# Kernel optimization log

Hardware: AMD Instinct MI355X
Metric: run time of the kernel (lower is better)

The kernel has to match this reference:

```python
import jax, jax.numpy as jnp
import numpy as np

N, E, D, H, HID = 50000, 400000, 64, 8, 1024
NEG_SLOPE = 0.2
BN_EPS = 1e-5


def setup_inputs() -> dict:
    key = jax.random.key(0)
    ks = jax.random.split(key, 10)
    s = 0.05
    return {
        "x": jax.random.normal(ks[0], (N, D), jnp.float32),
        "src": jax.random.randint(ks[1], (E,), 0, N, jnp.int32),
        "dst": jax.random.randint(ks[2], (E,), 0, N, jnp.int32),
        "fc_w": jax.random.normal(ks[3], (H * D, D), jnp.float32) * s,
        "attn_l": jax.random.normal(ks[4], (H, D), jnp.float32) * s,
        "attn_r": jax.random.normal(ks[5], (H, D), jnp.float32) * s,
        "gat_bias": jnp.zeros((H * D,), jnp.float32),
        "bn1_gamma": jnp.ones((H * D,), jnp.float32),
        "bn1_beta": jnp.zeros((H * D,), jnp.float32),
        "w1": jax.random.normal(ks[6], (HID, H * D), jnp.float32) * s,
        "b1": jnp.zeros((HID,), jnp.float32),
        "w2": jax.random.normal(ks[7], (D, HID), jnp.float32) * s,
        "b2": jnp.zeros((D,), jnp.float32),
        "bn2_gamma": jnp.ones((D,), jnp.float32),
        "bn2_beta": jnp.zeros((D,), jnp.float32),
    }


def _batchnorm(h, gamma, beta):
    # training-mode BatchNorm1d: batch statistics over node axis
    mu = h.mean(axis=0)
    var = h.var(axis=0)
    return gamma * (h - mu) * jax.lax.rsqrt(var + BN_EPS) + beta


def reference(x, src, dst, fc_w, attn_l, attn_r, gat_bias,
              bn1_gamma, bn1_beta, w1, b1, w2, b2, bn2_gamma, bn2_beta):
    n = x.shape[0]
    nh, dh = attn_l.shape
    # --- GATConv ---
    feat = (x @ fc_w.T).reshape(n, nh, dh)                 # [N,H,Dh]
    el = jnp.einsum("nhd,hd->nh", feat, attn_l)            # [N,H]
    er = jnp.einsum("nhd,hd->nh", feat, attn_r)            # [N,H]
    e = jax.nn.leaky_relu(el[src] + er[dst], NEG_SLOPE)    # [E,H]
    # edge softmax grouped by destination node (numerically stable)
    emax = jax.ops.segment_max(e, dst, num_segments=n)
    emax = jnp.where(jnp.isfinite(emax), emax, 0.0)        # nodes w/ no in-edges
    ez = jnp.exp(e - emax[dst])
    denom = jax.ops.segment_sum(ez, dst, num_segments=n)
    alpha = ez / denom[dst]                                # [E,H]
    msg = alpha[:, :, None] * feat[src]                    # [E,H,Dh]
    rst = jax.ops.segment_sum(msg, dst, num_segments=n)    # [N,H,Dh]
    rst = rst + gat_bias.reshape(nh, dh)
    h = rst.reshape(n, nh * dh)                            # flatten(1)
    # --- feed forward: BN -> Linear -> ReLU -> Linear -> BN ---
    h = _batchnorm(h, bn1_gamma, bn1_beta)
    h = jax.nn.relu(h @ w1.T + b1)
    h = h @ w2.T + b2
    h = _batchnorm(h, bn2_gamma, bn2_beta)
    return h
```

## Files before the change

kernel.cpp:

```cpp
#include <hip/hip_runtime.h>

#define NEG_SLOPE 0.2f
#define BN_EPS 1e-5f

typedef __bf16 bf16x8 __attribute__((ext_vector_type(8)));
typedef float  f32x4  __attribute__((ext_vector_type(4)));
typedef unsigned short ushort8_t __attribute__((ext_vector_type(8)));

__device__ __forceinline__ unsigned short f2bf(float f) {
    unsigned int u = __float_as_uint(f);
    unsigned int r = u + 0x7FFFu + ((u >> 16) & 1u);
    return (unsigned short)(r >> 16);
}
__device__ __forceinline__ float bf2f(unsigned short u) {
    return __uint_as_float(((unsigned int)u) << 16);
}
__device__ __forceinline__ void gload16(const void* g, void* l) {
    __builtin_amdgcn_global_load_lds(
        (const __attribute__((address_space(1))) unsigned int*)g,
        (__attribute__((address_space(3))) unsigned int*)l, 16, 0, 0);
}

__global__ __launch_bounds__(256)
void prep(const float* __restrict__ x, const int* __restrict__ dst,
          const float* __restrict__ fc_w, const float* __restrict__ w2,
          const float* __restrict__ attn_l, const float* __restrict__ attn_r,
          unsigned short* __restrict__ xbf, unsigned short* __restrict__ fcwbf,
          unsigned short* __restrict__ w2bf, float* __restrict__ proj,
          int* __restrict__ counts, int totX4, int E,
          int bCvtx, int bHist, int bFcw, int bW2)
{
    const int bid = blockIdx.x, tid = threadIdx.x;
    if (bid < bCvtx) {
        int i4 = bid * 256 + tid;
        if (i4 < totX4) {
            float4 v = *(const float4*)(x + (size_t)i4 * 4);
            ushort4 o = {f2bf(v.x), f2bf(v.y), f2bf(v.z), f2bf(v.w)};
            *(ushort4*)(xbf + (size_t)i4 * 4) = o;
        }
    } else if (bid < bHist) {
        int base = (bid - bCvtx) * 1024 + tid;
        #pragma unroll
        for (int k = 0; k < 4; ++k) {
            int e = base + k * 256;
            if (e < E) atomicAdd(&counts[dst[e]], 1);
        }
    } else if (bid < bFcw) {
        int i4 = (bid - bHist) * 256 + tid;
        if (i4 < 8192) {
            float4 v = *(const float4*)(fc_w + (size_t)i4 * 4);
            ushort4 o = {f2bf(v.x), f2bf(v.y), f2bf(v.z), f2bf(v.w)};
            *(ushort4*)(fcwbf + (size_t)i4 * 4) = o;
        }
    } else if (bid < bW2) {
        int i4 = (bid - bFcw) * 256 + tid;
        if (i4 < 16384) {
            float4 v = *(const float4*)(w2 + (size_t)i4 * 4);
            ushort4 o = {f2bf(v.x), f2bf(v.y), f2bf(v.z), f2bf(v.w)};
            *(ushort4*)(w2bf + (size_t)i4 * 4) = o;
        }
    } else {
        for (int t2 = tid; t2 < 512; t2 += 256) {
            int h = t2 >> 6, k = t2 & 63;
            float al = 0.f, ar = 0.f;
            for (int d = 0; d < 64; ++d) {
                float w = fc_w[(size_t)(h * 64 + d) * 64 + k];
                al = fmaf(attn_l[h * 64 + d], w, al);
                ar = fmaf(attn_r[h * 64 + d], w, ar);
            }
            proj[t2] = al;
            proj[512 + t2] = ar;
        }
    }
}

__global__ __launch_bounds__(256)
void scan1_elr(const int* __restrict__ counts, int* __restrict__ incl,
               int* __restrict__ bsum, int N, int NB,
               const float* __restrict__ x, const float* __restrict__ proj,
               float* __restrict__ el, float* __restrict__ er, int NH)
{
    __shared__ int sm[256];
    if ((int)blockIdx.x < NB) {
        int i = blockIdx.x * 256 + threadIdx.x;
        int v = (i < N) ? counts[i] : 0;
        sm[threadIdx.x] = v;
        __syncthreads();
        #pragma unroll
        for (int d = 1; d < 256; d <<= 1) {
            int t = (threadIdx.x >= d) ? sm[threadIdx.x - d] : 0;
            __syncthreads();
            sm[threadIdx.x] += t;
            __syncthreads();
        }
        if (i < N) incl[i] = sm[threadIdx.x];
        if (threadIdx.x == 255) bsum[blockIdx.x] = sm[255];
    } else {
        int idx = (blockIdx.x - NB) * 256 + threadIdx.x;
        if (idx >= NH) return;
        int h = idx & 7, n = idx >> 3;
        const float4* f  = (const float4*)(x + (size_t)n * 64);
        const float4* pl = (const float4*)(proj + h * 64);
        const float4* pr = (const float4*)(proj + 512 + h * 64);
        float sl = 0.f, sr = 0.f;
        #pragma unroll
        for (int i = 0; i < 16; ++i) {
            float4 fv = f[i], lv = pl[i], rv = pr[i];
            sl += fv.x * lv.x + fv.y * lv.y + fv.z * lv.z + fv.w * lv.w;
            sr += fv.x * rv.x + fv.y * rv.y + fv.z * rv.z + fv.w * rv.w;
        }
        el[idx] = sl;
        er[idx] = sr;
    }
}

__global__ void scan23(const int* __restrict__ incl, const int* __restrict__ bsum,
                       int* __restrict__ row_ptr, int* __restrict__ cursor, int N, int NB)
{
    __shared__ int sm[256];
    int t = threadIdx.x;
    sm[t] = (t < (int)blockIdx.x && t < NB) ? bsum[t] : 0;
    __syncthreads();
    #pragma unroll
    for (int d = 128; d > 0; d >>= 1) {
        if (t < d) sm[t] += sm[t + d];
        __syncthreads();
    }
    int pre = sm[0];
    int i = blockIdx.x * 256 + t;
    if (i < N) {
        int v = incl[i] + pre;
        row_ptr[i + 1] = v;
        cursor[i + 1] = v;
    }
    if (i == 0) { row_ptr[0] = 0; cursor[0] = 0; }
}

__global__ void scatter_edges(const int* __restrict__ src, const int* __restrict__ dst,
                              int* __restrict__ cursor, int* __restrict__ esrc, int E) {
    int e = blockIdx.x * 256 + threadIdx.x;
    if (e < E) {
        int p = atomicAdd(&cursor[dst[e]], 1);
        esrc[p] = src[e];
    }
}

__global__ __launch_bounds__(256)
void gat_aggregate(const int* __restrict__ row_ptr, const int* __restrict__ esrc,
                   const float* __restrict__ el, const float* __restrict__ er,
                   const unsigned short* __restrict__ xb, unsigned short* __restrict__ xagg,
                   int N)
{
    int node = blockIdx.x * 4 + (threadIdx.x >> 6);
    if (node >= N) return;
    const int lane = threadIdx.x & 63;
    const int h = lane >> 3, j = lane & 7;
    const int beg = row_ptr[node], end = row_ptr[node + 1];
    const float er_n = er[node * 8 + h];

    float denom = 0.f;
    float a[8] = {};
    int s_cur = (beg < end) ? esrc[beg] : 0;
    for (int k = beg; k < end; ++k) {
        int s_nxt = (k + 1 < end) ? esrc[k + 1] : 0;
        float elv = el[s_cur * 8 + h];
        ushort8_t fv = *(const ushort8_t*)(xb + (size_t)s_cur * 64 + j * 8);
        float v = elv + er_n;
        v = (v > 0.f) ? v : NEG_SLOPE * v;
        float z = __expf(v);
        denom += z;
        #pragma unroll
        for (int t = 0; t < 8; ++t) a[t] = fmaf(z, bf2f(fv[t]), a[t]);
        s_cur = s_nxt;
    }
    float inv = (end > beg) ? 1.f / denom : 0.f;
    ushort8_t o;
    #pragma unroll
    for (int t = 0; t < 8; ++t) o[t] = f2bf(a[t] * inv);
    *(ushort8_t*)(xagg + (size_t)node * 512 + lane * 8) = o;
}

__global__ __launch_bounds__(256)
void bn1_stats(const unsigned short* __restrict__ Xa,
               const unsigned short* __restrict__ Fw,
               const float* __restrict__ gat_bias,
               float* __restrict__ sums1, int M)
{
    __shared__ alignas(16) char Asm[128 * 64 * 2];
    __shared__ alignas(16) char Bsm[64 * 64 * 2];
    __shared__ float reds[4][64], redq[4][64];
    const int tid = threadIdx.x, lane = tid & 63, wave = tid >> 6;
    const int bm = blockIdx.x * 128;
    const int head = blockIdx.y;
    const int lr = lane >> 3, lk = ((lane & 7) ^ lr) * 8;

    #pragma unroll
    for (int it = 0; it < 4; ++it) {
        int seg = wave * 4 + it;
        gload16(Xa + (size_t)(bm + seg * 8 + lr) * 512 + head * 64 + lk, Asm + seg * 1024);
    }
    #pragma unroll
    for (int it = 0; it < 2; ++it) {
        int seg = wave * 2 + it;
        gload16(Fw + (size_t)(head * 64 + seg * 8 + lr) * 64 + lk, Bsm + seg * 1024);
    }
    __syncthreads();

    f32x4 acc[2][4] = {};
    #pragma unroll
    for (int kk = 0; kk < 2; ++kk) {
        int kg = kk * 4 + (lane >> 4);
        bf16x8 a[2], b[4];
        #pragma unroll
        for (int i = 0; i < 2; ++i) {
            int row = wave * 32 + i * 16 + (lane & 15);
            a[i] = *(const bf16x8*)(Asm + row * 128 + ((kg ^ (row & 7)) << 4));
        }
        #pragma unroll
        for (int j = 0; j < 4; ++j) {
            int row = j * 16 + (lane & 15);
            b[j] = *(const bf16x8*)(Bsm + row * 128 + ((kg ^ (row & 7)) << 4));
        }
        #pragma unroll
        for (int i = 0; i < 2; ++i)
            #pragma unroll
            for (int j = 0; j < 4; ++j)
                acc[i][j] = __builtin_amdgcn_mfma_f32_16x16x32_bf16(a[i], b[j], acc[i][j], 0, 0, 0);
    }

    float s4[4] = {}, q4[4] = {};
    #pragma unroll
    for (int j = 0; j < 4; ++j) {
        int col = j * 16 + (lane & 15);
        float bias = gat_bias[head * 64 + col];
        #pragma unroll
        for (int i = 0; i < 2; ++i)
            #pragma unroll
            for (int r = 0; r < 4; ++r) {
                int gm = bm + wave * 32 + i * 16 + (lane >> 4) * 4 + r;
                if (gm < M) {
                    float vq = bf2f(f2bf(acc[i][j][r] + bias));
                    s4[j] += vq; q4[j] += vq * vq;
                }
            }
    }
    #pragma unroll
    for (int j = 0; j < 4; ++j) {
        s4[j] += __shfl_xor(s4[j], 16); q4[j] += __shfl_xor(q4[j], 16);
        s4[j] += __shfl_xor(s4[j], 32); q4[j] += __shfl_xor(q4[j], 32);
    }
    if (lane < 16) {
        #pragma unroll
        for (int j = 0; j < 4; ++j) {
            reds[wave][j * 16 + lane] = s4[j];
            redq[wave][j * 16 + lane] = q4[j];
        }
    }
    __syncthreads();
    if (wave == 0 && lane < 16) {
        #pragma unroll
        for (int j = 0; j < 4; ++j) {
            int c = j * 16 + lane;
            atomicAdd(&sums1[head * 64 + c], reds[0][c] + reds[1][c] + reds[2][c] + reds[3][c]);
            atomicAdd(&sums1[512 + head * 64 + c], redq[0][c] + redq[1][c] + redq[2][c] + redq[3][c]);
        }
    }
}

__global__ __launch_bounds__(256)
void fold(const float* __restrict__ w1, const float* __restrict__ fc_w,
          const float* __restrict__ sums1, const float* __restrict__ gamma,
          const float* __restrict__ beta, const float* __restrict__ gat_bias,
          const float* __restrict__ b1, unsigned short* __restrict__ wtil,
          float* __restrict__ b1p, float invM)
{
    const int bid = blockIdx.x, tid = threadIdx.x;
    if (bid < 64) {
        __shared__ float sF[64][65];
        __shared__ float sa[64];
        int ot = bid >> 3, h = bid & 7;
        if (tid < 64) {
            int c = h * 64 + tid;
            float mu = sums1[c] * invM;
            float var = sums1[512 + c] * invM - mu * mu;
            sa[tid] = gamma[c] * rsqrtf(var + BN_EPS);
        }
        for (int e = 0; e < 16; ++e) {
            int idx = tid * 16 + e;
            int d = idx >> 6, k = idx & 63;
            sF[k][d] = fc_w[(size_t)(h * 64 + d) * 64 + k];
        }
        __syncthreads();
        int ol = tid >> 1, half = tid & 1;
        int o = ot * 128 + ol;
        int kbase = half * 32;
        float acc[32];
        #pragma unroll
        for (int i = 0; i < 32; ++i) acc[i] = 0.f;
        const float* wrow = w1 + (size_t)o * 512 + h * 64;
        #pragma unroll
        for (int dc = 0; dc < 4; ++dc) {
            float wa[16];
            #pragma unroll
            for (int d = 0; d < 16; ++d) wa[d] = wrow[dc * 16 + d] * sa[dc * 16 + d];
            #pragma unroll
            for (int kk2 = 0; kk2 < 32; ++kk2) {
                float s = acc[kk2];
                #pragma unroll
                for (int d = 0; d < 16; ++d) s = fmaf(wa[d], sF[kbase + kk2][dc * 16 + d], s);
                acc[kk2] = s;
            }
        }
        unsigned int* orow = (unsigned int*)(wtil + (size_t)o * 512 + h * 64 + kbase);
        #pragma unroll
        for (int i = 0; i < 16; ++i)
            orow[i] = (unsigned int)f2bf(acc[2 * i]) | ((unsigned int)f2bf(acc[2 * i + 1]) << 16);
    } else {
        __shared__ float ss[512];
        for (int c = tid; c < 512; c += 256) {
            float mu = sums1[c] * invM;
            float var = sums1[512 + c] * invM - mu * mu;
            float a = gamma[c] * rsqrtf(var + BN_EPS);
            ss[c] = beta[c] + a * (gat_bias[c] - mu);
        }
        __syncthreads();
        int wave = tid >> 6, lane = tid & 63;
        int o = (bid - 64) * 4 + wave;
        const float* wrow = w1 + (size_t)o * 512 + lane * 8;
        float p = 0.f;
        #pragma unroll
        for (int t2 = 0; t2 < 8; ++t2) p = fmaf(wrow[t2], ss[lane * 8 + t2], p);
        #pragma unroll
        for (int d = 1; d < 64; d <<= 1) p += __shfl_xor(p, d);
        if (lane == 0) b1p[o] = b1[o] + p;
    }
}

__global__ __launch_bounds__(256)
void gemm2p(const unsigned short* __restrict__ A,
            const unsigned short* __restrict__ B,
            const unsigned short* __restrict__ W2,
            const float* __restrict__ b1p,
            unsigned short* __restrict__ P,
            int M)
{
    __shared__ alignas(16) char smem[49152];
    char* Abuf0 = smem;
    char* Abuf1 = smem + 16384;
    char* Bbuf  = smem + 32768;
    char* TR   = smem;
    char* Wbuf = smem + 32768;
    char* PK   = smem + 32768;

    const int tid = threadIdx.x, lane = tid & 63, wave = tid >> 6;
    const int wr = wave >> 1, wc = wave & 1;
    const int lr = lane >> 3, lk = ((lane & 7) ^ lr) * 8;

    int bid = blockIdx.x;
    int wgid = (bid & 7) * 391 + (bid >> 3);
    const int bm = (wgid >> 3) * 128;
    const int t  = wgid & 7;
    const int bn = t * 128;

    #pragma unroll
    for (int it = 0; it < 4; ++it) {
        int seg = wave * 4 + it;
        gload16(A + (size_t)(bm + seg * 8 + lr) * 512 + lk, Abuf0 + seg * 1024);
    }

    f32x4 acc[4][4] = {};
    #pragma unroll
    for (int ks = 0; ks < 8; ++ks) {
        const int k0 = ks * 64;
        #pragma unroll
        for (int it = 0; it < 4; ++it) {
            int seg = wave * 4 + it;
            gload16(B + (size_t)(bn + seg * 8 + lr) * 512 + k0 + lk, Bbuf + seg * 1024);
        }
        if (ks < 7) {
            char* An = (ks & 1) ? Abuf0 : Abuf1;
            #pragma unroll
            for (int it = 0; it < 4; ++it) {
                int seg = wave * 4 + it;
                gload16(A + (size_t)(bm + seg * 8 + lr) * 512 + (k0 + 64) + lk, An + seg * 1024);
            }
            asm volatile("s_waitcnt vmcnt(4)" ::: "memory");
        } else {
            asm volatile("s_waitcnt vmcnt(0)" ::: "memory");
        }
        __builtin_amdgcn_s_barrier();
        __builtin_amdgcn_sched_barrier(0);
        const char* Ac = (ks & 1) ? Abuf1 : Abuf0;
        #pragma unroll
        for (int kk = 0; kk < 2; ++kk) {
            int kg = kk * 4 + (lane >> 4);
            bf16x8 a[4], b[4];
            #pragma unroll
            for (int i = 0; i < 4; ++i) {
                int row = wr * 64 + i * 16 + (lane & 15);
                a[i] = *(const bf16x8*)(Ac + row * 128 + ((kg ^ (row & 7)) << 4));
            }
            #pragma unroll
            for (int j = 0; j < 4; ++j) {
                int row = wc * 64 + j * 16 + (lane & 15);
                b[j] = *(const bf16x8*)(Bbuf + row * 128 + ((kg ^ (row & 7)) << 4));
            }
            #pragma unroll
            for (int i = 0; i < 4; ++i)
                #pragma unroll
                for (int j = 0; j < 4; ++j)
                    acc[i][j] = __builtin_amdgcn_mfma_f32_16x16x32_bf16(a[i], b[j], acc[i][j], 0, 0, 0);
        }
        __builtin_amdgcn_sched_barrier(0);
        __builtin_amdgcn_s_barrier();
        __builtin_amdgcn_sched_barrier(0);
    }

    #pragma unroll
    for (int j = 0; j < 4; ++j) {
        int c = wc * 64 + j * 16 + (lane & 15);
        float bs = b1p[bn + c];
        #pragma unroll
        for (int i = 0; i < 4; ++i)
            #pragma unroll
            for (int r = 0; r < 4; ++r) {
                int rw = wr * 64 + i * 16 + (lane >> 4) * 4 + r;
                float v = fmaxf(acc[i][j][r] + bs, 0.f);
                *(unsigned short*)(TR + rw * 256 + (((c >> 3) ^ (rw & 7)) << 4) + (c & 7) * 2) = f2bf(v);
            }
    }
    #pragma unroll
    for (int it = 0; it < 4; ++it) {
        int oc = wave * 16 + it * 4 + (lane >> 4);
        int g = lane & 15;
        gload16(W2 + (size_t)oc * 1024 + bn + ((g ^ (oc & 7))) * 8, Wbuf + (wave * 4 + it) * 1024);
    }
    __syncthreads();

    f32x4 pacc[2][4] = {};
    #pragma unroll
    for (int ks = 0; ks < 4; ++ks) {
        int kg2 = ks * 4 + (lane >> 4);
        #pragma unroll
        for (int i = 0; i < 2; ++i) {
            int arow = wave * 32 + i * 16 + (lane & 15);
            bf16x8 av = *(const bf16x8*)(TR + arow * 256 + ((kg2 ^ (arow & 7)) << 4));
            #pragma unroll
            for (int j = 0; j < 4; ++j) {
                int oc = j * 16 + (lane & 15);
                bf16x8 bv = *(const bf16x8*)(Wbuf + oc * 256 + ((kg2 ^ (oc & 7)) << 4));
                pacc[i][j] = __builtin_amdgcn_mfma_f32_16x16x32_bf16(av, bv, pacc[i][j], 0, 0, 0);
            }
        }
    }
    __syncthreads();

    #pragma unroll
    for (int i = 0; i < 2; ++i)
        #pragma unroll
        for (int j = 0; j < 4; ++j)
            #pragma unroll
            for (int r = 0; r < 4; ++r) {
                int row = wave * 32 + i * 16 + (lane >> 4) * 4 + r;
                int col = j * 16 + (lane & 15);
                *(unsigned short*)(PK + row * 128 + col * 2) = f2bf(pacc[i][j][r]);
            }
    __syncthreads();
    unsigned short* Pt = P + (size_t)t * M * 64;
    #pragma unroll
    for (int it = 0; it < 4; ++it) {
        int u = it * 256 + tid;
        int row = u >> 3, g8 = u & 7;
        int gm = bm + row;
        if (gm < M) {
            uint4 v = *(const uint4*)(PK + row * 128 + g8 * 16);
            *(uint4*)(Pt + (size_t)gm * 64 + g8 * 8) = v;
        }
    }
}

__global__ __launch_bounds__(256)
void reduce_bn2(const unsigned short* __restrict__ P, const float* __restrict__ b2,
                float* __restrict__ out, int M, float* __restrict__ sums2)
{
    __shared__ float ls[256], lq[256];
    int c = threadIdx.x & 63, g = threadIdx.x >> 6;
    const size_t S = (size_t)M * 64;
    float bias = b2[c];
    float s = 0.f, q = 0.f;
    for (int r = blockIdx.x * 4 + g; r < M; r += gridDim.x * 4) {
        size_t idx = (size_t)r * 64 + c;
        float v = bias;
        #pragma unroll
        for (int t = 0; t < 8; ++t) v += bf2f(P[t * S + idx]);
        out[idx] = v;
        s += v; q += v * v;
    }
    ls[threadIdx.x] = s; lq[threadIdx.x] = q;
    __syncthreads();
    if (g == 0) {
        s = ls[c] + ls[64 + c] + ls[128 + c] + ls[192 + c];
        q = lq[c] + lq[64 + c] + lq[128 + c] + lq[192 + c];
        atomicAdd(&sums2[c], s);
        atomicAdd(&sums2[64 + c], q);
    }
}

__global__ __launch_bounds__(256)
void bn_apply64(float* __restrict__ X, const float* __restrict__ sums2,
                const float* __restrict__ gamma, const float* __restrict__ beta,
                int M, float invM)
{
    int c = threadIdx.x & 63, g = threadIdx.x >> 6;
    float mu = sums2[c] * invM;
    float var = sums2[64 + c] * invM - mu * mu;
    float a = gamma[c] * rsqrtf(var + BN_EPS);
    float b = beta[c] - a * mu;
    for (int r = blockIdx.x * 4 + g; r < M; r += gridDim.x * 4) {
        size_t i = (size_t)r * 64 + c;
        X[i] = fmaf(a, X[i], b);
    }
}

extern "C" void kernel_launch(void* const* d_in, const int* in_sizes, int n_in,
                              void* d_out, int out_size, void* d_ws, size_t ws_size,
                              hipStream_t stream)
{
    const float* x         = (const float*)d_in[0];
    const int*   src       = (const int*)d_in[1];
    const int*   dst       = (const int*)d_in[2];
    const float* fc_w      = (const float*)d_in[3];
    const float* attn_l    = (const float*)d_in[4];
    const float* attn_r    = (const float*)d_in[5];
    const float* gat_bias  = (const float*)d_in[6];
    const float* bn1_gamma = (const float*)d_in[7];
    const float* bn1_beta  = (const float*)d_in[8];
    const float* w1        = (const float*)d_in[9];
    const float* b1        = (const float*)d_in[10];
    const float* w2        = (const float*)d_in[11];
    const float* b2        = (const float*)d_in[12];
    const float* bn2_gamma = (const float*)d_in[13];
    const float* bn2_beta  = (const float*)d_in[14];
    float* out = (float*)d_out;

    const int D = 64, HD = 512, HID = 1024;
    const int N = in_sizes[0] / D;
    const int E = in_sizes[1];
    const int NH = N * 8;
    const int NB = (N + 255) / 256;
    const int Mpad = ((N + 127) / 128) * 128 + 128;

    size_t off = 0;
    auto alloc = [&](size_t bytes) -> void* {
        void* p = (char*)d_ws + off;
        off += (bytes + 255) & ~(size_t)255;
        return p;
    };
    unsigned short* xagg = (unsigned short*)alloc((size_t)Mpad * HD * 2);
    unsigned short* P    = (unsigned short*)alloc((size_t)8 * N * D * 2);
    unsigned short* xbf  = (unsigned short*)alloc((size_t)N * D * 2);
    unsigned short* fcwbf = (unsigned short*)alloc((size_t)HD * D * 2);
    unsigned short* wtil = (unsigned short*)alloc((size_t)HID * HD * 2);
    unsigned short* w2bf = (unsigned short*)alloc((size_t)D * HID * 2);
    float* b1p   = (float*)alloc(HID * 4);
    float* proj  = (float*)alloc(2 * 512 * 4);
    float* el    = (float*)alloc((size_t)NH * 4);
    float* er    = (float*)alloc((size_t)NH * 4);
    char* zbase  = (char*)d_ws + off;
    int* counts  = (int*)alloc((size_t)N * 4);
    float* sums1 = (float*)alloc(2 * 512 * 4);
    float* sums2 = (float*)alloc(2 * 64 * 4);
    size_t zbytes = ((char*)d_ws + off) - zbase;
    int* incl    = (int*)alloc((size_t)N * 4);
    int* row_ptr = (int*)alloc((size_t)(N + 1) * 4);
    int* cursor  = (int*)alloc((size_t)(N + 1) * 4);
    int* bsum    = (int*)alloc(256 * 4);
    int* esrc    = (int*)alloc((size_t)E * 4);
    (void)ws_size; (void)n_in; (void)out_size;

    hipMemsetAsync(zbase, 0, zbytes, stream);

    {
        int totX4 = (N * D) / 4;
        int bCvtx = (totX4 + 255) / 256;
        int bHist = bCvtx + (E + 1023) / 1024;
        int bFcw  = bHist + 32;
        int bW2   = bFcw + 64;
        int grid  = bW2 + 1;
        prep<<<grid, 256, 0, stream>>>(x, dst, fc_w, w2, attn_l, attn_r,
                                       xbf, fcwbf, w2bf, proj, counts,
                                       totX4, E, bCvtx, bHist, bFcw, bW2);
    }

    scan1_elr<<<NB + (NH + 255) / 256, 256, 0, stream>>>(counts, incl, bsum, N, NB,
                                                         x, proj, el, er, NH);
    scan23<<<NB, 256, 0, stream>>>(incl, bsum, row_ptr, cursor, N, NB);
    scatter_edges<<<(E + 255) / 256, 256, 0, stream>>>(src, dst, cursor, esrc, E);

    gat_aggregate<<<(N + 3) / 4, 256, 0, stream>>>(row_ptr, esrc, el, er, xbf, xagg, N);

    {
        dim3 grid((N + 127) / 128, 8);
        bn1_stats<<<grid, 256, 0, stream>>>(xagg, fcwbf, gat_bias, sums1, N);
    }
    fold<<<320, 256, 0, stream>>>(w1, fc_w, sums1, bn1_gamma, bn1_beta, gat_bias,
                                  b1, wtil, b1p, 1.f / N);

    {
        int nwg = ((N + 127) / 128) * 8;
        gemm2p<<<nwg, 256, 0, stream>>>(xagg, wtil, w2bf, b1p, P, N);
    }

    reduce_bn2<<<1024, 256, 0, stream>>>(P, b2, out, N, sums2);
    bn_apply64<<<1024, 256, 0, stream>>>(out, sums2, bn2_gamma, bn2_beta, N, 1.f / N);
}
```

Measured before the change: 294.5 us.

## Fuse two-pass scan into single-pass decoupled lookback and read bf16 x for el/er

Merges the scan kernels into one launch. Each scan block publishes its block sum with a flag bit, then spins on earlier blocks' flagged sums to form its prefix, removing the incl buffer and a kernel launch. The el/er projection now reads the bf16 copy of x instead of fp32, halving that read traffic at some precision cost. Progress relies on earlier blocks being scheduled before later ones spin; the spin is bounded by NB ≤ 256 blocks.

```diff
diff --git a/kernel.cpp b/kernel.cpp
--- a/kernel.cpp
+++ b/kernel.cpp
@@ -75,13 +75,14 @@
 }
 
 __global__ __launch_bounds__(256)
-void scan1_elr(const int* __restrict__ counts, int* __restrict__ incl,
-               int* __restrict__ bsum, int N, int NB,
-               const float* __restrict__ x, const float* __restrict__ proj,
-               float* __restrict__ el, float* __restrict__ er, int NH)
-{
-    __shared__ int sm[256];
+void scan_elr(const int* __restrict__ counts, int* __restrict__ bsum,
+              int* __restrict__ row_ptr, int* __restrict__ cursor, int N, int NB,
+              const unsigned short* __restrict__ xbf, const float* __restrict__ proj,
+              float* __restrict__ el, float* __restrict__ er, int NH)
+{
     if ((int)blockIdx.x < NB) {
+        __shared__ int sm[256];
+        __shared__ int rm[256];
         int i = blockIdx.x * 256 + threadIdx.x;
         int v = (i < N) ? counts[i] : 0;
         sm[threadIdx.x] = v;
@@ -93,47 +94,49 @@
             sm[threadIdx.x] += t;
             __syncthreads();
         }
-        if (i < N) incl[i] = sm[threadIdx.x];
-        if (threadIdx.x == 255) bsum[blockIdx.x] = sm[255];
+        if (threadIdx.x == 255)
+            atomicExch(&bsum[blockIdx.x], sm[255] | 0x40000000);
+        int myagg = 0;
+        if ((int)threadIdx.x < (int)blockIdx.x) {
+            int vv;
+            do { vv = atomicAdd(&bsum[threadIdx.x], 0); } while (!(vv & 0x40000000));
+            myagg = vv & 0x3FFFFFFF;
+        }
+        rm[threadIdx.x] = myagg;
+        __syncthreads();
+        #pragma unroll
+        for (int d = 128; d > 0; d >>= 1) {
+            if (threadIdx.x < d) rm[threadIdx.x] += rm[threadIdx.x + d];
+            __syncthreads();
+        }
+        int pre = rm[0];
+        if (i < N) {
+            int w = sm[threadIdx.x] + pre;
+            row_ptr[i + 1] = w;
+            cursor[i + 1] = w;
+        }
+        if (i == 0) { row_ptr[0] = 0; cursor[0] = 0; }
     } else {
         int idx = (blockIdx.x - NB) * 256 + threadIdx.x;
         if (idx >= NH) return;
         int h = idx & 7, n = idx >> 3;
-        const float4* f  = (const float4*)(x + (size_t)n * 64);
-        const float4* pl = (const float4*)(proj + h * 64);
-        const float4* pr = (const float4*)(proj + 512 + h * 64);
+        const ushort8_t* f = (const ushort8_t*)(xbf + (size_t)n * 64);
+        const float* pl = proj + h * 64;
+        const float* pr = proj + 512 + h * 64;
         float sl = 0.f, sr = 0.f;
         #pragma unroll
-        for (int i = 0; i < 16; ++i) {
-            float4 fv = f[i], lv = pl[i], rv = pr[i];
-            sl += fv.x * lv.x + fv.y * lv.y + fv.z * lv.z + fv.w * lv.w;
-            sr += fv.x * rv.x + fv.y * rv.y + fv.z * rv.z + fv.w * rv.w;
+        for (int i8 = 0; i8 < 8; ++i8) {
+            ushort8_t v = f[i8];
+            #pragma unroll
+            for (int t = 0; t < 8; ++t) {
+                float fv = bf2f(v[t]);
+                sl = fmaf(fv, pl[i8 * 8 + t], sl);
+                sr = fmaf(fv, pr[i8 * 8 + t], sr);
+            }
         }
         el[idx] = sl;
         er[idx] = sr;
     }
-}
-
-__global__ void scan23(const int* __restrict__ incl, const int* __restrict__ bsum,
-                       int* __restrict__ row_ptr, int* __restrict__ cursor, int N, int NB)
-{
-    __shared__ int sm[256];
-    int t = threadIdx.x;
-    sm[t] = (t < (int)blockIdx.x && t < NB) ? bsum[t] : 0;
-    __syncthreads();
-    #pragma unroll
-    for (int d = 128; d > 0; d >>= 1) {
-        if (t < d) sm[t] += sm[t + d];
-        __syncthreads();
-    }
-    int pre = sm[0];
-    int i = blockIdx.x * 256 + t;
-    if (i < N) {
-        int v = incl[i] + pre;
-        row_ptr[i + 1] = v;
-        cursor[i + 1] = v;
-    }
-    if (i == 0) { row_ptr[0] = 0; cursor[0] = 0; }
 }
 
 __global__ void scatter_edges(const int* __restrict__ src, const int* __restrict__ dst,
@@ -570,11 +573,10 @@
     int* counts  = (int*)alloc((size_t)N * 4);
     float* sums1 = (float*)alloc(2 * 512 * 4);
     float* sums2 = (float*)alloc(2 * 64 * 4);
+    int* bsum    = (int*)alloc(256 * 4);
     size_t zbytes = ((char*)d_ws + off) - zbase;
-    int* incl    = (int*)alloc((size_t)N * 4);
     int* row_ptr = (int*)alloc((size_t)(N + 1) * 4);
     int* cursor  = (int*)alloc((size_t)(N + 1) * 4);
-    int* bsum    = (int*)alloc(256 * 4);
     int* esrc    = (int*)alloc((size_t)E * 4);
     (void)ws_size; (void)n_in; (void)out_size;
 
@@ -592,9 +594,8 @@
                                        totX4, E, bCvtx, bHist, bFcw, bW2);
     }
 
-    scan1_elr<<<NB + (NH + 255) / 256, 256, 0, stream>>>(counts, incl, bsum, N, NB,
-                                                         x, proj, el, er, NH);
-    scan23<<<NB, 256, 0, stream>>>(incl, bsum, row_ptr, cursor, N, NB);
+    scan_elr<<<NB + (NH + 255) / 256, 256, 0, stream>>>(counts, bsum, row_ptr, cursor,
+                                                        N, NB, xbf, proj, el, er, NH);
     scatter_edges<<<(E + 255) / 256, 256, 0, stream>>>(src, dst, cursor, esrc, E);
 
     gat_aggregate<<<(N + 3) / 4, 256, 0, stream>>>(row_ptr, esrc, el, er, xbf, xagg, N);
```

Result: no change. 291.1 us (median of 2 runs) (-1.1%).
